# Performance work log

Hardware: AMD Instinct MI355X
Metric: run time of the kernel (lower is better)

## Reference

```python
import jax, jax.numpy as jnp
import numpy as np

B, T = 1, 2048
N_EMBD = 4096
N_HEAD = 32
N_GROUPS = 8
HEAD = 128
Q_PER_KV = N_HEAD // N_GROUPS  # 4
WINDOW = 1024
EPS = 1e-5
ROPE_THETA = 10000.0


def setup_inputs() -> dict:
    key = jax.random.key(0)
    k0, k1, k2 = jax.random.split(key, 3)
    x = jax.random.normal(k0, (B, T, N_EMBD), dtype=jnp.float32)
    # RoPE tables: cos/sin of shape [T, HEAD] (rotary_percentage=1.0)
    inv_freq = 1.0 / (ROPE_THETA ** (jnp.arange(0, HEAD, 2, dtype=jnp.float32) / HEAD))
    ang = jnp.arange(T, dtype=jnp.float32)[:, None] * inv_freq[None, :]  # [T, HEAD//2]
    ang = jnp.concatenate([ang, ang], axis=-1)  # [T, HEAD]
    cos, sin = jnp.cos(ang), jnp.sin(ang)
    qkv_out = (N_HEAD + 2 * N_GROUPS) * HEAD  # 6144
    W_qkv = jax.random.normal(k1, (qkv_out, N_EMBD), dtype=jnp.float32) * 0.02
    W_proj = jax.random.normal(k2, (N_EMBD, N_HEAD * HEAD), dtype=jnp.float32) * 0.02
    norm_q_w = jnp.ones((N_HEAD * HEAD,), dtype=jnp.float32)
    norm_k_w = jnp.ones((N_GROUPS * HEAD,), dtype=jnp.float32)
    return {"x": x, "cos": cos, "sin": sin, "W_qkv": W_qkv,
            "norm_q_w": norm_q_w, "norm_k_w": norm_k_w, "W_proj": W_proj}


def _rmsnorm(x, w):
    # RMSNorm over last dim, matching litgpt RMSNorm (eps inside sqrt)
    var = jnp.mean(x * x, axis=-1, keepdims=True)
    return x * jax.lax.rsqrt(var + EPS) * w


def _apply_rope(x, cos, sin):
    # x: [B, H, T, D]; cos/sin: [T, D] (broadcast over B, H)
    d = x.shape[-1]
    x1, x2 = x[..., : d // 2], x[..., d // 2:]
    rotated = jnp.concatenate([-x2, x1], axis=-1)
    return x * cos + rotated * sin


def reference(x, cos, sin, W_qkv, norm_q_w, norm_k_w, W_proj):
    Bx, Tx, _ = x.shape
    qkv = jnp.einsum('btc,oc->bto', x, W_qkv)  # [B, T, (H+2G)*D]
    q_size = N_HEAD * HEAD
    kv_size = N_GROUPS * HEAD
    q = qkv[..., :q_size]
    k = qkv[..., q_size:q_size + kv_size]
    v = qkv[..., q_size + kv_size:]
    # norm_qk: RMSNorm over the full flattened q / k dims (pre head reshape)
    q = _rmsnorm(q, norm_q_w)
    k = _rmsnorm(k, norm_k_w)
    q = q.reshape(Bx, Tx, N_HEAD, HEAD).transpose(0, 2, 1, 3)     # [B, H, T, D]
    k = k.reshape(Bx, Tx, N_GROUPS, HEAD).transpose(0, 2, 1, 3)   # [B, G, T, D]
    v = v.reshape(Bx, Tx, N_GROUPS, HEAD).transpose(0, 2, 1, 3)   # [B, G, T, D]
    # rope_n_elem == head_size (rotary_percentage = 1.0)
    q = _apply_rope(q, cos, sin)
    k = _apply_rope(k, cos, sin)
    # GQA: expand kv groups to heads (repeat_interleave on head dim)
    k = jnp.repeat(k, Q_PER_KV, axis=1)  # [B, H, T, D]
    v = jnp.repeat(v, Q_PER_KV, axis=1)
    scale = 1.0 / jnp.sqrt(jnp.float32(HEAD))  # attention_scores_scalar is None
    scores = jnp.einsum('bhqd,bhkd->bhqk', q, k) * scale
    # causal + sliding-window mask: allowed iff 0 <= q_idx - kv_idx < WINDOW
    d = jnp.arange(Tx)[:, None] - jnp.arange(Tx)[None, :]
    bias = jnp.where((d >= 0) & (d < WINDOW), 0.0, -jnp.inf).astype(scores.dtype)
    attn = jax.nn.softmax(scores + bias, axis=-1)
    y = jnp.einsum('bhqk,bhkd->bhqd', attn, v)        # [B, H, T, D]
    y = y.transpose(0, 2, 1, 3).reshape(Bx, Tx, N_HEAD * HEAD)
    return jnp.einsum('bth,oh->bto', y, W_proj)       # [B, T, n_embd]
```

## Files before the change

kernel.cpp:

```cpp
#include <hip/hip_runtime.h>
#include <stdint.h>
#include <stddef.h>

#define T_SEQ 2048
#define WINDOW_SZ 1024

typedef __attribute__((ext_vector_type(4))) float f32x4;
typedef __attribute__((ext_vector_type(16))) float f32x16;
typedef __attribute__((ext_vector_type(8))) short s16x8;
typedef __attribute__((ext_vector_type(4))) short s16x4;

__device__ inline unsigned short f2bf(float f) {
  union { float f; unsigned u; } v; v.f = f;
  unsigned u = v.u;
  return (unsigned short)((u + 0x7fffu + ((u >> 16) & 1u)) >> 16);
}
__device__ inline float bf2f(unsigned short u) {
  union { unsigned u; float f; } v; v.u = ((unsigned)u) << 16; return v.f;
}

__device__ inline void gld_lds16(const unsigned short* g, unsigned short* l) {
  __builtin_amdgcn_global_load_lds((const __attribute__((address_space(1))) void*)g,
                                   (__attribute__((address_space(3))) void*)l, 16, 0, 0);
}

__device__ inline void store_out(float* p, float v) { *p = v; }
__device__ inline void store_out(unsigned short* p, float v) { *p = f2bf(v); }

__global__ __launch_bounds__(256) void cvt_all(const float* __restrict__ x,
                                               const float* __restrict__ wqkv,
                                               const float* __restrict__ wproj,
                                               unsigned short* __restrict__ x_bf,
                                               unsigned short* __restrict__ wqkv_bf,
                                               unsigned short* __restrict__ wproj_bf) {
  int i = blockIdx.x * 256 + threadIdx.x;
  const float* s; unsigned short* d; int j;
  if (i < 2097152)       { s = x;     d = x_bf;     j = i; }
  else if (i < 8388608)  { s = wqkv;  d = wqkv_bf;  j = i - 2097152; }
  else                   { s = wproj; d = wproj_bf; j = i - 8388608; }
  float4 v = ((const float4*)s)[j];
  ushort4 o;
  o.x = f2bf(v.x); o.y = f2bf(v.y); o.z = f2bf(v.z); o.w = f2bf(v.w);
  ((ushort4*)d)[j] = o;
}

template <typename OutT>
__global__ __launch_bounds__(256) void gemm_bt(const unsigned short* __restrict__ A,
                                               const unsigned short* __restrict__ Bt,
                                               OutT* __restrict__ C, int M, int N, int K) {
  __shared__ unsigned short As[128 * 64];
  __shared__ unsigned short Bs[128 * 64];
  const int tid  = threadIdx.x;
  const int wave = tid >> 6, lane = tid & 63;
  const int l32 = lane & 31, khalf = lane >> 5;
  const int m0 = blockIdx.y << 7, n0 = blockIdx.x << 7;
  const int wr = (wave >> 1) << 6;
  const int wc = (wave & 1) << 6;
  const int srow = wave * 8 + (lane >> 3);
  const int gchunk0 = lane & 7;

  f32x16 acc[2][2] = {};

  for (int k0 = 0; k0 < K; k0 += 64) {
#pragma unroll
    for (int j = 0; j < 4; j++) {
      int r = j * 32 + srow;
      int gc = gchunk0 ^ (r & 7);
      gld_lds16(A  + (size_t)(m0 + r) * K + k0 + gc * 8, &As[(j * 32 + wave * 8) * 64]);
      gld_lds16(Bt + (size_t)(n0 + r) * K + k0 + gc * 8, &Bs[(j * 32 + wave * 8) * 64]);
    }
    __syncthreads();
#pragma unroll
    for (int s = 0; s < 4; s++) {
      s16x8 af[2], bfr[2];
      int chunk = s * 2 + khalf;
#pragma unroll
      for (int i = 0; i < 2; i++) {
        int ra = wr + i * 32 + l32;
        af[i]  = *(const s16x8*)&As[ra * 64 + ((chunk ^ (ra & 7)) * 8)];
        int rb = wc + i * 32 + l32;
        bfr[i] = *(const s16x8*)&Bs[rb * 64 + ((chunk ^ (rb & 7)) * 8)];
      }
#pragma unroll
      for (int mi = 0; mi < 2; mi++)
#pragma unroll
        for (int ni = 0; ni < 2; ni++)
          acc[mi][ni] = __builtin_amdgcn_mfma_f32_32x32x16_bf16(af[mi], bfr[ni], acc[mi][ni], 0, 0, 0);
    }
    __syncthreads();
  }
#pragma unroll
  for (int mi = 0; mi < 2; mi++)
#pragma unroll
    for (int ni = 0; ni < 2; ni++) {
      int col = n0 + wc + ni * 32 + l32;
      int rbase = m0 + wr + mi * 32 + 4 * khalf;
#pragma unroll
      for (int reg = 0; reg < 16; reg++) {
        int row = rbase + (reg & 3) + 8 * (reg >> 2);
        store_out(&C[(size_t)row * N + col], acc[mi][ni][reg]);
      }
    }
}

__global__ __launch_bounds__(256) void normrope(const unsigned short* __restrict__ qkv,
                                                const float* __restrict__ cosb,
                                                const float* __restrict__ sinb,
                                                const float* __restrict__ wq,
                                                const float* __restrict__ wk,
                                                unsigned short* __restrict__ qr,
                                                unsigned short* __restrict__ kr,
                                                unsigned short* __restrict__ vt) {
  const int t = blockIdx.x, tid = threadIdx.x;
  const unsigned short* row = qkv + (size_t)t * 6144;
  float sq = 0.f, sk = 0.f;
  {
    s16x8 a = *(const s16x8*)&row[tid * 16];
    s16x8 b = *(const s16x8*)&row[tid * 16 + 8];
#pragma unroll
    for (int j = 0; j < 8; j++) {
      float fa = bf2f((unsigned short)a[j]), fb = bf2f((unsigned short)b[j]);
      sq += fa * fa + fb * fb;
    }
  }
  {
    s16x4 a = *(const s16x4*)&row[4096 + tid * 4];
#pragma unroll
    for (int j = 0; j < 4; j++) {
      float fa = bf2f((unsigned short)a[j]);
      sk += fa * fa;
    }
  }
#pragma unroll
  for (int off = 32; off; off >>= 1) { sq += __shfl_xor(sq, off); sk += __shfl_xor(sk, off); }
  __shared__ float red[8];
  if ((tid & 63) == 0) { red[tid >> 6] = sq; red[4 + (tid >> 6)] = sk; }
  __syncthreads();
  sq = red[0] + red[1] + red[2] + red[3];
  sk = red[4] + red[5] + red[6] + red[7];
  const float rq = rsqrtf(sq * (1.f / 4096.f) + 1e-5f) * (0.08838834764831845f * 1.4426950408889634f);
  const float rk = rsqrtf(sk * (1.f / 1024.f) + 1e-5f);
  for (int i = tid; i < 4096; i += 256) {
    int h = i >> 7, d = i & 127;
    int pd = (d < 64) ? d + 64 : d - 64;
    float val = bf2f(row[i]) * rq * wq[i];
    float pv  = bf2f(row[(h << 7) + pd]) * rq * wq[(h << 7) + pd];
    float rot = (d < 64) ? -pv : pv;
    float o = val * cosb[t * 128 + d] + rot * sinb[t * 128 + d];
    qr[(size_t)h * T_SEQ * 128 + t * 128 + d] = f2bf(o);
  }
  for (int i = tid; i < 1024; i += 256) {
    int g = i >> 7, d = i & 127;
    int pd = (d < 64) ? d + 64 : d - 64;
    float val = bf2f(row[4096 + i]) * rk * wk[i];
    float pv  = bf2f(row[4096 + (g << 7) + pd]) * rk * wk[(g << 7) + pd];
    float rot = (d < 64) ? -pv : pv;
    float o = val * cosb[t * 128 + d] + rot * sinb[t * 128 + d];
    kr[(size_t)g * T_SEQ * 128 + t * 128 + d] = f2bf(o);
  }
  for (int i = tid; i < 1024; i += 256) {
    int g = i >> 7, d = i & 127;
    vt[(size_t)g * 128 * T_SEQ + (size_t)d * T_SEQ + t] = row[5120 + i];
  }
}

__global__ __launch_bounds__(512, 2) void attn(const unsigned short* __restrict__ Q,
                                               const unsigned short* __restrict__ Kb,
                                               const unsigned short* __restrict__ Vt,
                                               unsigned short* __restrict__ Y) {
  __shared__ unsigned short Kbuf[2][64 * 128];
  __shared__ unsigned short Vbuf[2][128 * 64];
  __shared__ unsigned short Pbuf[8][2][16 * 72];
  const int qb = blockIdx.x, g = blockIdx.y;
  const int tid = threadIdx.x, wave = tid >> 6, lane = tid & 63;
  const int quad = lane >> 4, l16 = lane & 15;
  const int h = g * 4 + (wave >> 1);
  const int qbase = qb * 64;
  const int q0 = qbase + (wave & 1) * 32;
  const unsigned short* Qh = Q + (size_t)h * T_SEQ * 128;
  const unsigned short* Kg = Kb + (size_t)g * T_SEQ * 128;
  const unsigned short* Vg = Vt + (size_t)g * 128 * T_SEQ;

  s16x8 aq[2][4];
#pragma unroll
  for (int qt = 0; qt < 2; qt++)
#pragma unroll
    for (int ks = 0; ks < 4; ks++)
      aq[qt][ks] = *(const s16x8*)&Qh[(size_t)(q0 + qt * 16 + l16) * 128 + ks * 32 + quad * 8];

  f32x4 acc[2][8] = {};
  float lrow[2][4] = {};

  int lo = qbase - (WINDOW_SZ - 1);
  if (lo < 0) lo = 0;
  lo &= ~63;

#define STAGE_CHUNK(buf, kkv)                                                        \
  {                                                                                  \
    int kk_ = (kkv);                                                                 \
    _Pragma("unroll")                                                                \
    for (int j = 0; j < 2; j++) {                                                    \
      int rloc = wave * 8 + j * 4 + (lane >> 4);                                     \
      int oct = (lane & 15) ^ (rloc & 15);                                           \
      gld_lds16(Kg + (size_t)(kk_ + rloc) * 128 + oct * 8,                           \
                &Kbuf[buf][(wave * 8 + j * 4) * 128]);                               \
    }                                                                                \
    _Pragma("unroll")                                                                \
    for (int j = 0; j < 2; j++) {                                                    \
      int dloc = wave * 16 + j * 8 + (lane >> 3);                                    \
      int oct = (lane & 7) ^ (dloc & 7);                                             \
      gld_lds16(Vg + (size_t)dloc * T_SEQ + kk_ + oct * 8,                           \
                &Vbuf[buf][(wave * 16 + j * 8) * 64]);                               \
    }                                                                                \
  }

  STAGE_CHUNK(0, lo);
  int ib = 0;
  for (int kk = lo; kk < qbase + 64; kk += 64, ib ^= 1) {
    __syncthreads();
    if (kk + 64 < qbase + 64) STAGE_CHUNK(ib ^ 1, kk + 64);
    if (kk > q0 + 31 || kk + 63 < q0 - (WINDOW_SZ - 1)) continue;
    const unsigned short* kb = Kbuf[ib];
    const unsigned short* vb = Vbuf[ib];
    f32x4 sc[2][4] = {};
#pragma unroll
    for (int ks = 0; ks < 4; ks++) {
#pragma unroll
      for (int ci = 0; ci < 4; ci++) {
        s16x8 bk = *(const s16x8*)&kb[(ci * 16 + l16) * 128 + (((ks * 4 + quad) ^ l16) * 8)];
        sc[0][ci] = __builtin_amdgcn_mfma_f32_16x16x32_bf16(aq[0][ks], bk, sc[0][ci], 0, 0, 0);
        sc[1][ci] = __builtin_amdgcn_mfma_f32_16x16x32_bf16(aq[1][ks], bk, sc[1][ci], 0, 0, 0);
      }
    }
#pragma unroll
    for (int qt = 0; qt < 2; qt++)
#pragma unroll
      for (int ci = 0; ci < 4; ci++) {
        int col = kk + ci * 16 + l16;
#pragma unroll
        for (int r = 0; r < 4; r++) {
          int irow = q0 + qt * 16 + quad * 4 + r;
          unsigned dd = (unsigned)(irow - col);
          float e = (dd < (unsigned)WINDOW_SZ) ? exp2f(sc[qt][ci][r]) : 0.f;
          lrow[qt][r] += e;
          Pbuf[wave][qt][(quad * 4 + r) * 72 + ci * 16 + l16] = f2bf(e);
        }
      }
#pragma unroll
    for (int c = 0; c < 2; c++) {
      s16x8 pa0 = *(const s16x8*)&Pbuf[wave][0][l16 * 72 + c * 32 + quad * 8];
      s16x8 pa1 = *(const s16x8*)&Pbuf[wave][1][l16 * 72 + c * 32 + quad * 8];
#pragma unroll
      for (int n = 0; n < 8; n++) {
        s16x8 bv = *(const s16x8*)&vb[(n * 16 + l16) * 64 + (((c * 4 + quad) ^ (l16 & 7)) * 8)];
        acc[0][n] = __builtin_amdgcn_mfma_f32_16x16x32_bf16(pa0, bv, acc[0][n], 0, 0, 0);
        acc[1][n] = __builtin_amdgcn_mfma_f32_16x16x32_bf16(pa1, bv, acc[1][n], 0, 0, 0);
      }
    }
  }
#undef STAGE_CHUNK
#pragma unroll
  for (int qt = 0; qt < 2; qt++)
#pragma unroll
    for (int r = 0; r < 4; r++) {
#pragma unroll
      for (int off = 8; off; off >>= 1) lrow[qt][r] += __shfl_xor(lrow[qt][r], off);
      lrow[qt][r] = 1.f / lrow[qt][r];
    }
#pragma unroll
  for (int qt = 0; qt < 2; qt++)
#pragma unroll
    for (int n = 0; n < 8; n++)
#pragma unroll
      for (int r = 0; r < 4; r++) {
        int irow = q0 + qt * 16 + quad * 4 + r;
        Y[(size_t)irow * 4096 + h * 128 + n * 16 + l16] = f2bf(acc[qt][n][r] * lrow[qt][r]);
      }
}

extern "C" void kernel_launch(void* const* d_in, const int* in_sizes, int n_in,
                              void* d_out, int out_size, void* d_ws, size_t ws_size,
                              hipStream_t stream) {
  (void)in_sizes; (void)n_in; (void)out_size; (void)ws_size;
  const float* x     = (const float*)d_in[0];
  const float* cosb  = (const float*)d_in[1];
  const float* sinb  = (const float*)d_in[2];
  const float* Wqkv  = (const float*)d_in[3];
  const float* wq    = (const float*)d_in[4];
  const float* wk    = (const float*)d_in[5];
  const float* Wproj = (const float*)d_in[6];
  float* out = (float*)d_out;

  char* ws = (char*)d_ws;
  unsigned short* x_bf     = (unsigned short*)(ws);
  unsigned short* wqkv_bf  = (unsigned short*)(ws + 16777216);
  unsigned short* wproj_bf = (unsigned short*)(ws + 67108864);
  unsigned short* qkv      = (unsigned short*)(ws + 100663296);
  unsigned short* qr       = (unsigned short*)(ws + 150994944);
  unsigned short* kr       = (unsigned short*)(ws + 167772160);
  unsigned short* vt       = (unsigned short*)(ws + 171966464);
  unsigned short* y        = (unsigned short*)(ws + 176160768);

  cvt_all<<<49152, 256, 0, stream>>>(x, Wqkv, Wproj, x_bf, wqkv_bf, wproj_bf);
  gemm_bt<unsigned short><<<dim3(48, 16), 256, 0, stream>>>(x_bf, wqkv_bf, qkv, 2048, 6144, 4096);
  normrope<<<2048, 256, 0, stream>>>(qkv, cosb, sinb, wq, wk, qr, kr, vt);
  attn<<<dim3(32, 8), 512, 0, stream>>>(qr, kr, vt, y);
  gemm_bt<float><<<dim3(32, 16), 256, 0, stream>>>(y, wproj_bf, out, 2048, 4096, 4096);
}
```

Measured before the change: 503.6 us.

## Add 256x256-tile pipelined GEMM for QKV projection and MFMA priority hints

Replaces the QKV projection GEMM with a new 512-thread kernel that computes 256x256 output tiles. It double-buffers LDS and interleaves global-to-LDS staging of the next K slices with MFMA phases, using s_setprio to favour the matrix ops. The aim is more data reuse per tile and better overlap of memory with compute. The grid shrinks to 192 blocks, which may underfill the 256 CUs, and the 128KB shared buffer limits occupancy. The attention kernel also gets s_setprio around its MFMA loops.

```diff
diff --git a/kernel.cpp b/kernel.cpp
--- a/kernel.cpp
+++ b/kernel.cpp
@@ -100,6 +100,103 @@
         int row = rbase + (reg & 3) + 8 * (reg >> 2);
         store_out(&C[(size_t)row * N + col], acc[mi][ni][reg]);
       }
+    }
+}
+
+__device__ inline void stage_half(const unsigned short* __restrict__ g, int ldk,
+                                  int grow0, int k0, unsigned short* lds,
+                                  int wave, int lane) {
+#pragma unroll
+  for (int j = 0; j < 2; j++) {
+    int rloc = j * 64 + wave * 8 + (lane >> 3);
+    int lc = (lane & 7) ^ (rloc & 7);
+    gld_lds16(g + (size_t)(grow0 + rloc) * ldk + k0 + lc * 8,
+              lds + (j * 64 + wave * 8) * 64);
+  }
+}
+
+__global__ __launch_bounds__(512, 2) void gemm256(const unsigned short* __restrict__ A,
+                                                  const unsigned short* __restrict__ Bt,
+                                                  unsigned short* __restrict__ C,
+                                                  int M, int N, int K) {
+  __shared__ unsigned short S[65536];
+  const int tid = threadIdx.x, wave = tid >> 6, lane = tid & 63;
+  const int quad = lane >> 4, l16 = lane & 15;
+  const int wm = wave >> 2, wn = wave & 3;
+  const int m0 = blockIdx.y << 8, n0 = blockIdx.x << 8;
+  const int NT = K >> 6;
+
+  f32x4 acc[8][4] = {};
+
+  stage_half(Bt, K, n0,       0, &S[16384],        wave, lane);
+  stage_half(Bt, K, n0 + 128, 0, &S[16384 + 8192], wave, lane);
+  stage_half(A,  K, m0,       0, &S[0],            wave, lane);
+  stage_half(A,  K, m0 + 128, 0, &S[8192],         wave, lane);
+  if (NT > 1) {
+    stage_half(Bt, K, n0,       64, &S[32768 + 16384],        wave, lane);
+    stage_half(Bt, K, n0 + 128, 64, &S[32768 + 16384 + 8192], wave, lane);
+  }
+  asm volatile("s_waitcnt vmcnt(4)" ::: "memory");
+  __builtin_amdgcn_s_barrier();
+  asm volatile("" ::: "memory");
+
+  for (int u = 0; u < NT; ++u) {
+    const int b = u & 1;
+    const unsigned short* Sa = &S[b * 32768];
+    const unsigned short* Sb = &S[b * 32768 + 16384];
+    s16x8 bfr[4][2];
+#pragma unroll
+    for (int p = 0; p < 4; ++p) {
+      s16x8 af[2][2];
+#pragma unroll
+      for (int f = 0; f < 2; f++)
+#pragma unroll
+        for (int ks = 0; ks < 2; ks++) {
+          int ra = wm * 128 + (p * 2 + f) * 16 + l16;
+          af[f][ks] = *(const s16x8*)&Sa[ra * 64 + (((ks * 4 + quad) ^ (ra & 7)) * 8)];
+        }
+      if (p == 0) {
+#pragma unroll
+        for (int nf = 0; nf < 4; nf++)
+#pragma unroll
+          for (int ks = 0; ks < 2; ks++) {
+            int rb = wn * 64 + nf * 16 + l16;
+            bfr[nf][ks] = *(const s16x8*)&Sb[rb * 64 + (((ks * 4 + quad) ^ (rb & 7)) * 8)];
+          }
+      }
+      if (p == 0 && u + 1 < NT) stage_half(A,  K, m0,       (u + 1) << 6, &S[(b ^ 1) * 32768],                wave, lane);
+      if (p == 1 && u + 1 < NT) stage_half(A,  K, m0 + 128, (u + 1) << 6, &S[(b ^ 1) * 32768 + 8192],         wave, lane);
+      if (p == 2 && u + 2 < NT) stage_half(Bt, K, n0,       (u + 2) << 6, &S[b * 32768 + 16384],              wave, lane);
+      if (p == 3 && u + 2 < NT) stage_half(Bt, K, n0 + 128, (u + 2) << 6, &S[b * 32768 + 16384 + 8192],       wave, lane);
+
+      asm volatile("" ::: "memory");
+      __builtin_amdgcn_s_barrier();
+      asm volatile("" ::: "memory");
+      __builtin_amdgcn_s_setprio(1);
+#pragma unroll
+      for (int f = 0; f < 2; f++)
+#pragma unroll
+        for (int nf = 0; nf < 4; nf++)
+#pragma unroll
+          for (int ks = 0; ks < 2; ks++)
+            acc[p * 2 + f][nf] = __builtin_amdgcn_mfma_f32_16x16x32_bf16(
+                af[f][ks], bfr[nf][ks], acc[p * 2 + f][nf], 0, 0, 0);
+      __builtin_amdgcn_s_setprio(0);
+      if (p == 3) asm volatile("s_waitcnt vmcnt(4)" ::: "memory");
+      asm volatile("" ::: "memory");
+      __builtin_amdgcn_s_barrier();
+      asm volatile("" ::: "memory");
+    }
+  }
+#pragma unroll
+  for (int mf = 0; mf < 8; mf++)
+#pragma unroll
+    for (int nf = 0; nf < 4; nf++) {
+      const int row0 = m0 + wm * 128 + mf * 16 + quad * 4;
+      const int col  = n0 + wn * 64 + nf * 16 + l16;
+#pragma unroll
+      for (int r = 0; r < 4; r++)
+        C[(size_t)(row0 + r) * N + col] = f2bf(acc[mf][nf][r]);
     }
 }
 
@@ -223,6 +320,7 @@
     const unsigned short* kb = Kbuf[ib];
     const unsigned short* vb = Vbuf[ib];
     f32x4 sc[2][4] = {};
+    __builtin_amdgcn_s_setprio(1);
 #pragma unroll
     for (int ks = 0; ks < 4; ks++) {
 #pragma unroll
@@ -232,6 +330,7 @@
         sc[1][ci] = __builtin_amdgcn_mfma_f32_16x16x32_bf16(aq[1][ks], bk, sc[1][ci], 0, 0, 0);
       }
     }
+    __builtin_amdgcn_s_setprio(0);
 #pragma unroll
     for (int qt = 0; qt < 2; qt++)
 #pragma unroll
@@ -246,6 +345,7 @@
           Pbuf[wave][qt][(quad * 4 + r) * 72 + ci * 16 + l16] = f2bf(e);
         }
       }
+    __builtin_amdgcn_s_setprio(1);
 #pragma unroll
     for (int c = 0; c < 2; c++) {
       s16x8 pa0 = *(const s16x8*)&Pbuf[wave][0][l16 * 72 + c * 32 + quad * 8];
@@ -257,6 +357,7 @@
         acc[1][n] = __builtin_amdgcn_mfma_f32_16x16x32_bf16(pa1, bv, acc[1][n], 0, 0, 0);
       }
     }
+    __builtin_amdgcn_s_setprio(0);
   }
 #undef STAGE_CHUNK
 #pragma unroll
@@ -302,7 +403,7 @@
   unsigned short* y        = (unsigned short*)(ws + 176160768);
 
   cvt_all<<<49152, 256, 0, stream>>>(x, Wqkv, Wproj, x_bf, wqkv_bf, wproj_bf);
-  gemm_bt<unsigned short><<<dim3(48, 16), 256, 0, stream>>>(x_bf, wqkv_bf, qkv, 2048, 6144, 4096);
+  gemm256<<<dim3(24, 8), 512, 0, stream>>>(x_bf, wqkv_bf, qkv, 2048, 6144, 4096);
   normrope<<<2048, 256, 0, stream>>>(qkv, cosb, sinb, wq, wk, qr, kr, vt);
   attn<<<dim3(32, 8), 512, 0, stream>>>(qr, kr, vt, y);
   gemm_bt<float><<<dim3(32, 16), 256, 0, stream>>>(y, wproj_bf, out, 2048, 4096, 4096);
```

Measured after the change: 494.9 us. Within noise of the previous version (-1.7%).
